# Kernel tuning notes

Measured on AMD Instinct MI355X. Metric: run time of the kernel, lower is better.

## Reference

```python
import jax, jax.numpy as jnp
import numpy as np

EPS = 1e-5   # F.instance_norm default eps
SIG = 10.0   # getGraphLap sig


def conv1(x, K):
    # x: (B, C, N), K: (O, I, kw); torch F.conv1d with 'same' padding
    p = (K.shape[-1] - 1) // 2
    return jax.lax.conv_general_dilated(
        x, K, window_strides=(1,), padding=[(p, p)],
        dimension_numbers=("NCH", "OIH", "NCH"))


def conv1T(x, K):
    # F.conv_transpose1d(x, K, padding=(kw-1)//2) == conv1d with swapped
    # in/out channels and spatially flipped kernel (stride 1, kw odd)
    Kt = jnp.flip(jnp.transpose(K, (1, 0, 2)), axis=-1)
    return conv1(x, Kt)


def avg_pool3s2(x):
    # F.avg_pool1d(x, 3, stride=2, padding=1), count_include_pad=True
    s = jax.lax.reduce_window(x, 0.0, jax.lax.add, (1, 1, 3), (1, 1, 2),
                              [(0, 0), (0, 0), (1, 1)])
    return s / 3.0


def instance_norm(z):
    mu = jnp.mean(z, axis=-1, keepdims=True)
    var = jnp.var(z, axis=-1, keepdims=True)  # biased, as in torch
    return (z - mu) * jax.lax.rsqrt(var + EPS)


def graph_lap(X, m):
    # X: (1, d, N) coords, m: (1, 1, N) mask -> (N, N) masked graph Laplacian
    Xs = X[0]                                             # (d, N)
    M = m.reshape(-1)                                     # (N,)
    Xn = Xs / (jnp.std(Xs, axis=1, keepdims=True, ddof=1) + 0.01)
    sq = jnp.sum(Xn * Xn, axis=0)                         # (N,)
    D = jnp.maximum(sq[None, :] + sq[:, None] - 2.0 * (Xn.T @ Xn), 0.0)
    We = jnp.exp(-D / SIG)
    L = jnp.diag(jnp.sum(We, axis=0)) - We
    L = jnp.outer(M, M) * L + jnp.diag(1.0 - M)
    return 0.5 * (L + L.T)


def graph_unet(x, X, m, Ks):
    xS = []
    mS = [m]
    Ls = [graph_lap(X, m)]
    # encoder / coarsening path
    for K in Ks:
        coarsen = K.shape[0] != K.shape[1]
        if coarsen:
            xS.append(x)
        z = instance_norm(mS[-1] * conv1(jnp.matmul(x, Ls[-1]), K))
        x = jax.nn.relu(z) if coarsen else x + jax.nn.relu(z)
        if coarsen:
            x = avg_pool3s2(x)
            m = avg_pool3s2(m)
            X = avg_pool3s2(X)
            mS.append(m)
            Ls.append(graph_lap(X, m))
    # decoder / refinement path
    n_scales = len(xS)
    for K in reversed(Ks):
        refine = K.shape[0] != K.shape[1]
        if refine:
            n_scales -= 1
            x = jnp.repeat(x, 2, axis=-1)  # F.interpolate nearest x2
            mS = mS[:-1]
            Ls = Ls[:-1]
        z = instance_norm(mS[-1] * conv1T(jnp.matmul(x, Ls[-1]), K))
        x = jax.nn.relu(z) if refine else x + jax.nn.relu(z)
        if refine:
            x = x + xS[n_scales]
    return x


def kernel_shapes(nLevels=3, nIn=32, nsmooth=2, stencil=9):
    shapes = []
    k = nIn
    for _ in range(nLevels):
        shapes += [(k, k, stencil)] * nsmooth
        shapes.append((2 * k, k, stencil))
        k *= 2
    shapes += [(k, k, stencil)] * nsmooth
    return shapes  # 11 kernels for (3, 32, 2)


def setup_inputs() -> dict:
    key = jax.random.key(0)
    ks = jax.random.split(key, 16)
    N = 4096
    inp = {
        "x": jax.random.normal(ks[0], (1, 32, N), jnp.float32),
        "X": jax.random.normal(ks[1], (1, 3, N), jnp.float32),
        "m": jnp.ones((1, 1, N), jnp.float32),
    }
    stdv = 1e-3
    for i, s in enumerate(kernel_shapes()):
        inp[f"K{i}"] = jax.random.uniform(ks[2 + i], s, jnp.float32, -stdv, stdv)
    return inp


def reference(x, X, m, K0, K1, K2, K3, K4, K5, K6, K7, K8, K9, K10):
    Ks = [K0, K1, K2, K3, K4, K5, K6, K7, K8, K9, K10]
    return graph_unet(x, X, m, Ks)
```

## Files before the change

kernel.cpp:

```cpp
#include <hip/hip_runtime.h>
#include <math.h>

typedef __attribute__((ext_vector_type(8))) short bf16x8;
typedef __attribute__((ext_vector_type(4))) float f32x4;

__device__ __forceinline__ ushort f2b(float f) {
    union { float f; unsigned u; } v; v.f = f;
    unsigned r = (v.u + 0x7FFFu + ((v.u >> 16) & 1u)) >> 16;
    return (ushort)r;
}
__device__ __forceinline__ float b2f(ushort h) {
    union { unsigned u; float f; } v; v.u = ((unsigned)h) << 16;
    return v.f;
}


__global__ __launch_bounds__(256) void k_prep(const float* __restrict__ X,
                                              float* __restrict__ Xn,
                                              float* __restrict__ sq, int N) {
    __shared__ double sh_s[256], sh_ss[256];
    __shared__ float sst[3];
    int t = threadIdx.x;
    for (int r = 0; r < 3; r++) {
        const float* row = X + (size_t)r * N;
        double s = 0.0, ss = 0.0;
        for (int i = t * 4; i < N; i += 1024) {
            float4 v = *(const float4*)(row + i);
            s += (double)v.x + (double)v.y + (double)v.z + (double)v.w;
            ss += (double)v.x * v.x + (double)v.y * v.y + (double)v.z * v.z + (double)v.w * v.w;
        }
        sh_s[t] = s; sh_ss[t] = ss; __syncthreads();
        for (int off = 128; off > 0; off >>= 1) {
            if (t < off) { sh_s[t] += sh_s[t + off]; sh_ss[t] += sh_ss[t + off]; }
            __syncthreads();
        }
        if (t == 0) {
            double mean = sh_s[0] / N;
            double var = (sh_ss[0] - mean * sh_s[0]) / (N - 1);
            if (var < 0.0) var = 0.0;
            sst[r] = 1.0f / ((float)sqrt(var) + 0.01f);
        }
        __syncthreads();
    }
    float s0 = sst[0], s1 = sst[1], s2 = sst[2];
    for (int i = t * 4; i < N; i += 1024) {
        float4 v0 = *(const float4*)(X + i);
        float4 v1 = *(const float4*)(X + N + i);
        float4 v2 = *(const float4*)(X + 2 * N + i);
        v0.x *= s0; v0.y *= s0; v0.z *= s0; v0.w *= s0;
        v1.x *= s1; v1.y *= s1; v1.z *= s1; v1.w *= s1;
        v2.x *= s2; v2.y *= s2; v2.z *= s2; v2.w *= s2;
        *(float4*)(Xn + i) = v0;
        *(float4*)(Xn + N + i) = v1;
        *(float4*)(Xn + 2 * N + i) = v2;
        float4 sv;
        sv.x = v0.x * v0.x + v1.x * v1.x + v2.x * v2.x;
        sv.y = v0.y * v0.y + v1.y * v1.y + v2.y * v2.y;
        sv.z = v0.z * v0.z + v1.z * v1.z + v2.z * v2.z;
        sv.w = v0.w * v0.w + v1.w * v1.w + v2.w * v2.w;
        *(float4*)(sq + i) = sv;
    }
}

template<int CPT>
__global__ __launch_bounds__(256) void k_lap(const float* __restrict__ Xn,
                                             const float* __restrict__ sq,
                                             const float* __restrict__ m,
                                             ushort* __restrict__ L, int N) {
    int i = blockIdx.x;
    int t = threadIdx.x;
    int T = blockDim.x;
    float a0 = Xn[i], a1 = Xn[N + i], a2 = Xn[2 * N + i];
    float si = sq[i];
    int j0 = t * CPT;
    float w[CPT];
    float psum = 0.f;
    #pragma unroll
    for (int q4 = 0; q4 < CPT / 4; q4++) {
        int j = j0 + q4 * 4;
        float4 x0 = *(const float4*)(Xn + j);
        float4 x1 = *(const float4*)(Xn + N + j);
        float4 x2 = *(const float4*)(Xn + 2 * N + j);
        float4 sv = *(const float4*)(sq + j);
        float D;
        D = fmaxf(si + sv.x - 2.f * (a0 * x0.x + a1 * x1.x + a2 * x2.x), 0.f);
        w[q4 * 4 + 0] = exp2f(-D * 0.14426950408889634f);
        D = fmaxf(si + sv.y - 2.f * (a0 * x0.y + a1 * x1.y + a2 * x2.y), 0.f);
        w[q4 * 4 + 1] = exp2f(-D * 0.14426950408889634f);
        D = fmaxf(si + sv.z - 2.f * (a0 * x0.z + a1 * x1.z + a2 * x2.z), 0.f);
        w[q4 * 4 + 2] = exp2f(-D * 0.14426950408889634f);
        D = fmaxf(si + sv.w - 2.f * (a0 * x0.w + a1 * x1.w + a2 * x2.w), 0.f);
        w[q4 * 4 + 3] = exp2f(-D * 0.14426950408889634f);
        psum += w[q4 * 4] + w[q4 * 4 + 1] + w[q4 * 4 + 2] + w[q4 * 4 + 3];
    }
    __shared__ float red[256];
    red[t] = psum; __syncthreads();
    for (int off = T >> 1; off > 0; off >>= 1) {
        if (t < off) red[t] += red[t + off];
        __syncthreads();
    }
    float d = red[0];
    float mi = m[i];
    ushort* Lo = L + (size_t)i * N + j0;
    #pragma unroll
    for (int q4 = 0; q4 < CPT / 4; q4++) {
        int j = j0 + q4 * 4;
        float4 mj = *(const float4*)(m + j);
        ushort o[4];
        float lv;
        lv = ((j + 0 == i) ? d : 0.f) - w[q4 * 4 + 0]; lv = mi * mj.x * lv; if (j + 0 == i) lv += 1.f - mj.x; o[0] = f2b(lv);
        lv = ((j + 1 == i) ? d : 0.f) - w[q4 * 4 + 1]; lv = mi * mj.y * lv; if (j + 1 == i) lv += 1.f - mj.y; o[1] = f2b(lv);
        lv = ((j + 2 == i) ? d : 0.f) - w[q4 * 4 + 2]; lv = mi * mj.z * lv; if (j + 2 == i) lv += 1.f - mj.z; o[2] = f2b(lv);
        lv = ((j + 3 == i) ? d : 0.f) - w[q4 * 4 + 3]; lv = mi * mj.w * lv; if (j + 3 == i) lv += 1.f - mj.w; o[3] = f2b(lv);
        *(ushort4*)(Lo + q4 * 4) = make_ushort4(o[0], o[1], o[2], o[3]);
    }
}

template<int MODE>
__global__ __launch_bounds__(256) void k_mmfT(const void* __restrict__ xsrc,
                                              const ushort* __restrict__ Lb,
                                              ushort* __restrict__ yt, int N, int C) {
    __shared__ float lds[4][64][4];
    int t = threadIdx.x;
    int wv = t >> 6, l = t & 63;
    int lrow = l & 15, lk = l >> 4;
    int j0 = blockIdx.x * 16;
    int c0 = blockIdx.y * 32;

    if (blockIdx.x == 0) {
        int row = t >> 5;
        int ch = c0 + (t & 31);
        int jj = (row < 4) ? row : N + row;
        yt[(size_t)jj * C + ch] = 0;
    }

    int kquart = N >> 2;
    size_t kbase = (size_t)wv * kquart + lk * 8;
    const ushort* bp = Lb + (size_t)(j0 + lrow) * N + kbase;
    f32x4 accA = (f32x4){0.f, 0.f, 0.f, 0.f};
    f32x4 accB = (f32x4){0.f, 0.f, 0.f, 0.f};
    if (MODE == 0) {
        const ushort* apA = (const ushort*)xsrc + (size_t)(c0 + lrow) * N + kbase;
        const ushort* apB = (const ushort*)xsrc + (size_t)(c0 + 16 + lrow) * N + kbase;
        for (int k0 = 0; k0 < kquart; k0 += 32) {
            bf16x8 b = *(const bf16x8*)(bp + k0);
            bf16x8 aA = *(const bf16x8*)(apA + k0);
            bf16x8 aB = *(const bf16x8*)(apB + k0);
            accA = __builtin_amdgcn_mfma_f32_16x16x32_bf16(aA, b, accA, 0, 0, 0);
            accB = __builtin_amdgcn_mfma_f32_16x16x32_bf16(aB, b, accB, 0, 0, 0);
        }
    } else if (MODE == 1) {
        const float* apA = (const float*)xsrc + (size_t)(c0 + lrow) * N + kbase;
        const float* apB = (const float*)xsrc + (size_t)(c0 + 16 + lrow) * N + kbase;
        for (int k0 = 0; k0 < kquart; k0 += 32) {
            bf16x8 b = *(const bf16x8*)(bp + k0);
            float4 f0 = *(const float4*)(apA + k0);
            float4 f1 = *(const float4*)(apA + k0 + 4);
            bf16x8 aA;
            aA[0] = (short)f2b(f0.x); aA[1] = (short)f2b(f0.y);
            aA[2] = (short)f2b(f0.z); aA[3] = (short)f2b(f0.w);
            aA[4] = (short)f2b(f1.x); aA[5] = (short)f2b(f1.y);
            aA[6] = (short)f2b(f1.z); aA[7] = (short)f2b(f1.w);
            float4 g0 = *(const float4*)(apB + k0);
            float4 g1 = *(const float4*)(apB + k0 + 4);
            bf16x8 aB;
            aB[0] = (short)f2b(g0.x); aB[1] = (short)f2b(g0.y);
            aB[2] = (short)f2b(g0.z); aB[3] = (short)f2b(g0.w);
            aB[4] = (short)f2b(g1.x); aB[5] = (short)f2b(g1.y);
            aB[6] = (short)f2b(g1.z); aB[7] = (short)f2b(g1.w);
            accA = __builtin_amdgcn_mfma_f32_16x16x32_bf16(aA, b, accA, 0, 0, 0);
            accB = __builtin_amdgcn_mfma_f32_16x16x32_bf16(aB, b, accB, 0, 0, 0);
        }
    } else {
        const ushort* apA = (const ushort*)xsrc + (size_t)(c0 + lrow) * (N >> 1) + (kbase >> 1);
        const ushort* apB = (const ushort*)xsrc + (size_t)(c0 + 16 + lrow) * (N >> 1) + (kbase >> 1);
        for (int k0 = 0; k0 < kquart; k0 += 32) {
            bf16x8 b = *(const bf16x8*)(bp + k0);
            ushort4 v = *(const ushort4*)(apA + (k0 >> 1));
            bf16x8 aA;
            aA[0] = (short)v.x; aA[1] = (short)v.x;
            aA[2] = (short)v.y; aA[3] = (short)v.y;
            aA[4] = (short)v.z; aA[5] = (short)v.z;
            aA[6] = (short)v.w; aA[7] = (short)v.w;
            ushort4 u = *(const ushort4*)(apB + (k0 >> 1));
            bf16x8 aB;
            aB[0] = (short)u.x; aB[1] = (short)u.x;
            aB[2] = (short)u.y; aB[3] = (short)u.y;
            aB[4] = (short)u.z; aB[5] = (short)u.z;
            aB[6] = (short)u.w; aB[7] = (short)u.w;
            accA = __builtin_amdgcn_mfma_f32_16x16x32_bf16(aA, b, accA, 0, 0, 0);
            accB = __builtin_amdgcn_mfma_f32_16x16x32_bf16(aB, b, accB, 0, 0, 0);
        }
    }
    #pragma unroll
    for (int g = 0; g < 2; g++) {
        #pragma unroll
        for (int r = 0; r < 4; r++) lds[wv][l][r] = (g == 0) ? accA[r] : accB[r];
        __syncthreads();
        if (t < 64) {
            int gg = t >> 4, j16 = t & 15;
            float s0 = lds[0][t][0] + lds[1][t][0] + lds[2][t][0] + lds[3][t][0];
            float s1 = lds[0][t][1] + lds[1][t][1] + lds[2][t][1] + lds[3][t][1];
            float s2 = lds[0][t][2] + lds[1][t][2] + lds[2][t][2] + lds[3][t][2];
            float s3 = lds[0][t][3] + lds[1][t][3] + lds[2][t][3] + lds[3][t][3];
            *(ushort4*)(yt + (size_t)(j0 + j16 + 4) * C + c0 + g * 16 + gg * 4) =
                make_ushort4(f2b(s0), f2b(s1), f2b(s2), f2b(s3));
        }
        __syncthreads();
    }
}

struct WMeta {
    const float* src[11];
    unsigned long long off_f[11];
    unsigned long long off_t[11];
    int ca[11];
    int cb[11];
};

__global__ __launch_bounds__(256) void k_wprep(WMeta meta, ushort* __restrict__ Wm) {
    int which = blockIdx.y;
    int a = meta.ca[which], b = meta.cb[which];
    int tot = a * b * 9;
    int idx = blockIdx.x * 256 + threadIdx.x;
    if (idx >= tot) return;
    int t = idx % 9;
    int oi = idx / 9;
    int i = oi % b;
    int o = oi / b;
    ushort h = f2b(meta.src[which][idx]);
    Wm[meta.off_f[which] + ((size_t)t * a + o) * b + i] = h;
    Wm[meta.off_t[which] + ((size_t)(8 - t) * b + i) * a + o] = h;
}

__global__ __launch_bounds__(256) void k_convM(const ushort* __restrict__ yt,
                                               const ushort* __restrict__ Wm,
                                               float* __restrict__ zm,
                                               const float* __restrict__ m,
                                               float2* __restrict__ sp,
                                               int C_in, int C_out, int N,
                                               int iters, int NP) {
    __shared__ float lds[4][64][4];
    int t = threadIdx.x;
    int wv = t >> 6, l = t & 63;
    int prow = l & 15, kq = l >> 4;
    int p00 = blockIdx.x * 32;
    int o0 = blockIdx.y * 16;
    int per = (iters + 3) >> 2;
    int it0 = wv * per;
    int it1 = min(iters, it0 + per);
    f32x4 accA = (f32x4){0.f, 0.f, 0.f, 0.f};
    f32x4 accB = (f32x4){0.f, 0.f, 0.f, 0.f};
    for (int it = it0; it < it1; it++) {
        int ks = it / 9;
        int tp = it - ks * 9;
        int kb = ks * 32 + kq * 8;
        bf16x8 a = *(const bf16x8*)(Wm + ((size_t)tp * C_out + o0 + prow) * C_in + kb);
        bf16x8 bA = *(const bf16x8*)(yt + (size_t)(p00 + prow + tp) * C_in + kb);
        bf16x8 bB = *(const bf16x8*)(yt + (size_t)(p00 + 16 + prow + tp) * C_in + kb);
        accA = __builtin_amdgcn_mfma_f32_16x16x32_bf16(a, bA, accA, 0, 0, 0);
        accB = __builtin_amdgcn_mfma_f32_16x16x32_bf16(a, bB, accB, 0, 0, 0);
    }
    float stsum[4] = {0.f, 0.f, 0.f, 0.f}, stss[4] = {0.f, 0.f, 0.f, 0.f};
    #pragma unroll
    for (int pg = 0; pg < 2; pg++) {
        int p0 = p00 + pg * 16;
        #pragma unroll
        for (int r = 0; r < 4; r++) lds[wv][l][r] = (pg == 0) ? accA[r] : accB[r];
        __syncthreads();
        if (t < 64) {
            int g = t >> 4, j16 = t & 15;
            int j = p0 + j16;
            float mj = m[j];
            #pragma unroll
            for (int r = 0; r < 4; r++) {
                float z = lds[0][t][r] + lds[1][t][r] + lds[2][t][r] + lds[3][t][r];
                z *= mj;
                zm[(size_t)(o0 + g * 4 + r) * N + j] = z;
                float zs = z, zz = z * z;
                #pragma unroll
                for (int mask = 1; mask < 16; mask <<= 1) {
                    zs += __shfl_xor(zs, mask);
                    zz += __shfl_xor(zz, mask);
                }
                stsum[r] += zs; stss[r] += zz;
            }
        }
        __syncthreads();
    }
    if (t < 64 && (t & 15) == 0) {
        int g = t >> 4;
        #pragma unroll
        for (int r = 0; r < 4; r++)
            sp[(size_t)(o0 + g * 4 + r) * NP + blockIdx.x] = make_float2(stsum[r], stss[r]);
    }
}

__global__ __launch_bounds__(256) void k_convC2(const float* __restrict__ zm,
                                                const float2* __restrict__ sp,
                                                const float* __restrict__ res,
                                                float* __restrict__ xout,
                                                ushort* __restrict__ xob, int N, int NP) {
    int o = blockIdx.y;
    int t = threadIdx.x;
    float2 pp = (t < NP) ? sp[(size_t)o * NP + t] : make_float2(0.f, 0.f);
    __shared__ float red[256], red2[256];
    red[t] = pp.x; red2[t] = pp.y;
    __syncthreads();
    for (int off = 128; off > 0; off >>= 1) {
        if (t < off) { red[t] += red[t + off]; red2[t] += red2[t + off]; }
        __syncthreads();
    }
    float mean = red[0] / N;
    float var = fmaxf(red2[0] / N - mean * mean, 0.f);
    float rs = rsqrtf(var + 1e-5f);
    int base = blockIdx.x * 512 + t * 2;
    float2 z = *(const float2*)(zm + (size_t)o * N + base);
    float v0 = fmaxf((z.x - mean) * rs, 0.f);
    float v1 = fmaxf((z.y - mean) * rs, 0.f);
    if (res) {
        float2 r = *(const float2*)(res + (size_t)o * N + base);
        v0 += r.x; v1 += r.y;
    }
    *(float2*)(xout + (size_t)o * N + base) = make_float2(v0, v1);
    if (xob) *(ushort2*)(xob + (size_t)o * N + base) = make_ushort2(f2b(v0), f2b(v1));
}

__global__ __launch_bounds__(256) void k_poolall(const float* __restrict__ z_in,
                                                 float* __restrict__ z_out,
                                                 ushort* __restrict__ zb_out, int Cz,
                                                 const float* __restrict__ m_in, float* __restrict__ m_out,
                                                 const float* __restrict__ X_in, float* __restrict__ X_out, int Nin) {
    int No = Nin >> 1;
    int idx = blockIdx.x * 256 + threadIdx.x;
    int total = (Cz + 4) * No;
    if (idx >= total) return;
    int r = idx / No, ii = idx - r * No;
    const float* src;
    if (r < Cz) {
        src = z_in + (size_t)r * Nin;
        float a = (ii > 0) ? src[2 * ii - 1] : 0.f;
        float v = (a + src[2 * ii] + src[2 * ii + 1]) * (1.f / 3.f);
        z_out[(size_t)r * No + ii] = v;
        zb_out[(size_t)r * No + ii] = f2b(v);
    } else if (r == Cz) {
        src = m_in;
        float a = (ii > 0) ? src[2 * ii - 1] : 0.f;
        m_out[ii] = (a + src[2 * ii] + src[2 * ii + 1]) * (1.f / 3.f);
    } else {
        src = X_in + (size_t)(r - Cz - 1) * Nin;
        float a = (ii > 0) ? src[2 * ii - 1] : 0.f;
        X_out[(size_t)(r - Cz - 1) * No + ii] = (a + src[2 * ii] + src[2 * ii + 1]) * (1.f / 3.f);
    }
}


extern "C" void kernel_launch(void* const* d_in, const int* in_sizes, int n_in,
                              void* d_out, int out_size, void* d_ws, size_t ws_size,
                              hipStream_t stream) {
    (void)in_sizes; (void)n_in; (void)out_size; (void)ws_size;
    const float* x_in = (const float*)d_in[0];
    const float* X0 = (const float*)d_in[1];
    const float* m0 = (const float*)d_in[2];
    const float* Kw[11];
    for (int i = 0; i < 11; i++) Kw[i] = (const float*)d_in[3 + i];
    float* out = (float*)d_out;
    float* ws = (float*)d_ws;

    const int Ns[4] = {4096, 2048, 1024, 512};
    const int KA[11] = {32, 32, 64, 64, 64, 128, 128, 128, 256, 256, 256};
    const int KB[11] = {32, 32, 32, 64, 64, 64, 128, 128, 128, 256, 256};

    size_t off = 0;
    auto alloc = [&](size_t n) { float* p = ws + off; off += (n + 63) & ~(size_t)63; return p; };
    ushort* Lb[4];
    Lb[0] = (ushort*)alloc(8388608); Lb[1] = (ushort*)alloc(2097152);
    Lb[2] = (ushort*)alloc(524288);  Lb[3] = (ushort*)alloc(131072);
    float* Xnb = alloc(3 * 4096);
    float* sqb = alloc(4096);
    float* spbuf = alloc(32768);
    float* zmbuf = alloc(262144);
    float* mlev[4];
    mlev[0] = const_cast<float*>(m0);
    mlev[1] = alloc(2048); mlev[2] = alloc(1024); mlev[3] = alloc(512);
    float* Xlev[4];
    Xlev[0] = const_cast<float*>(X0);
    Xlev[1] = alloc(3 * 2048); Xlev[2] = alloc(3 * 1024); Xlev[3] = alloc(3 * 512);
    float* pA[4], *pB[4], *xs[3];
    for (int l = 0; l < 4; l++) { pA[l] = alloc(131072); pB[l] = alloc(131072); }
    for (int l = 0; l < 3; l++) xs[l] = alloc(131072);
    float* zbig = alloc(262144);
    ushort* pAb[4], *pBb[4], *xsb[3];
    for (int l = 0; l < 4; l++) { pAb[l] = (ushort*)alloc(65536); pBb[l] = (ushort*)alloc(65536); }
    for (int l = 0; l < 3; l++) xsb[l] = (ushort*)alloc(65536);
    ushort* ytb = (ushort*)alloc(140000);
    ushort* Wm = (ushort*)alloc(1960000);

    size_t woff_f[11], woff_t[11];
    {
        size_t acc = 0;
        for (int k = 0; k < 11; k++) { woff_f[k] = acc; acc += (size_t)KA[k] * KB[k] * 9; }
        for (int k = 0; k < 11; k++) { woff_t[k] = acc; acc += (size_t)KA[k] * KB[k] * 9; }
    }

    {
        WMeta meta;
        for (int k = 0; k < 11; k++) {
            meta.src[k] = Kw[k];
            meta.off_f[k] = woff_f[k];
            meta.off_t[k] = woff_t[k];
            meta.ca[k] = KA[k];
            meta.cb[k] = KB[k];
        }
        k_wprep<<<dim3(2304, 11), 256, 0, stream>>>(meta, Wm);
    }

    auto build_lap = [&](int lvl) {
        int N = Ns[lvl];
        k_prep<<<1, 256, 0, stream>>>(Xlev[lvl], Xnb, sqb, N);
        if (N == 4096)      k_lap<16><<<N, 256, 0, stream>>>(Xnb, sqb, mlev[lvl], Lb[lvl], N);
        else if (N == 2048) k_lap<8><<<N, 256, 0, stream>>>(Xnb, sqb, mlev[lvl], Lb[lvl], N);
        else if (N == 1024) k_lap<4><<<N, 256, 0, stream>>>(Xnb, sqb, mlev[lvl], Lb[lvl], N);
        else                k_lap<4><<<N, 128, 0, stream>>>(Xnb, sqb, mlev[lvl], Lb[lvl], N);
    };

    auto matmul = [&](const void* xsrc, int C, int lvl, int mode) {
        int N = Ns[lvl];
        dim3 g(N / 16, C / 32);
        if (mode == 0)      k_mmfT<0><<<g, 256, 0, stream>>>(xsrc, Lb[lvl], ytb, N, C);
        else if (mode == 1) k_mmfT<1><<<g, 256, 0, stream>>>(xsrc, Lb[lvl], ytb, N, C);
        else                k_mmfT<2><<<g, 256, 0, stream>>>(xsrc, Lb[lvl], ytb, N, C);
    };

    auto conv = [&](int kidx, int lvl, const float* resv, float* ov, ushort* ovb,
                    int Cin, int Cout, int tr) {
        int N = Ns[lvl];
        int iters = (Cin / 32) * 9;
        int NP = N / 32;
        const ushort* wm = Wm + (tr ? woff_t[kidx] : woff_f[kidx]);
        k_convM<<<dim3(N / 32, Cout / 16), 256, 0, stream>>>(ytb, wm, zmbuf, mlev[lvl],
                                                             (float2*)spbuf, Cin, Cout, N, iters, NP);
        int NBs = N / 512;
        k_convC2<<<dim3(NBs, Cout), 256, 0, stream>>>(zmbuf, (const float2*)spbuf, resv, ov, ovb, N, NP);
    };

    auto poolall = [&](const float* z_in, float* z_out, ushort* zb_out, int Cz, int lvl_from) {
        int Nin = Ns[lvl_from];
        int No = Nin >> 1;
        int total = (Cz + 4) * No;
        k_poolall<<<(total + 255) / 256, 256, 0, stream>>>(z_in, z_out, zb_out, Cz,
                                                           mlev[lvl_from], mlev[lvl_from + 1],
                                                           Xlev[lvl_from], Xlev[lvl_from + 1], Nin);
    };

    build_lap(0);
    matmul(x_in, 32, 0, 1);    conv(0, 0, x_in, pA[0], pAb[0], 32, 32, 0);
    matmul(pAb[0], 32, 0, 0);  conv(1, 0, pA[0], xs[0], xsb[0], 32, 32, 0);
    matmul(xsb[0], 32, 0, 0);  conv(2, 0, nullptr, zbig, nullptr, 32, 64, 0);
    poolall(zbig, pA[1], pAb[1], 64, 0);
    build_lap(1);
    matmul(pAb[1], 64, 1, 0);  conv(3, 1, pA[1], pB[1], pBb[1], 64, 64, 0);
    matmul(pBb[1], 64, 1, 0);  conv(4, 1, pB[1], xs[1], xsb[1], 64, 64, 0);
    matmul(xsb[1], 64, 1, 0);  conv(5, 1, nullptr, zbig, nullptr, 64, 128, 0);
    poolall(zbig, pA[2], pAb[2], 128, 1);
    build_lap(2);
    matmul(pAb[2], 128, 2, 0); conv(6, 2, pA[2], pB[2], pBb[2], 128, 128, 0);
    matmul(pBb[2], 128, 2, 0); conv(7, 2, pB[2], xs[2], xsb[2], 128, 128, 0);
    matmul(xsb[2], 128, 2, 0); conv(8, 2, nullptr, zbig, nullptr, 128, 256, 0);
    poolall(zbig, pA[3], pAb[3], 256, 2);
    build_lap(3);
    matmul(pAb[3], 256, 3, 0); conv(9, 3, pA[3], pB[3], pBb[3], 256, 256, 0);
    matmul(pBb[3], 256, 3, 0); conv(10, 3, pB[3], pA[3], pAb[3], 256, 256, 0);

    matmul(pAb[3], 256, 3, 0); conv(10, 3, pA[3], pB[3], pBb[3], 256, 256, 1);
    matmul(pBb[3], 256, 3, 0); conv(9, 3, pB[3], pA[3], pAb[3], 256, 256, 1);

    matmul(pAb[3], 256, 2, 2); conv(8, 2, xs[2], pB[2], pBb[2], 256, 128, 1);
    matmul(pBb[2], 128, 2, 0); conv(7, 2, pB[2], pA[2], pAb[2], 128, 128, 1);
    matmul(pAb[2], 128, 2, 0); conv(6, 2, pA[2], pB[2], pBb[2], 128, 128, 1);

    matmul(pBb[2], 128, 1, 2); conv(5, 1, xs[1], pA[1], pAb[1], 128, 64, 1);
    matmul(pAb[1], 64, 1, 0);  conv(4, 1, pA[1], pB[1], pBb[1], 64, 64, 1);
    matmul(pBb[1], 64, 1, 0);  conv(3, 1, pB[1], pA[1], pAb[1], 64, 64, 1);

    matmul(pAb[1], 64, 0, 2);  conv(2, 0, xs[0], pB[0], pBb[0], 64, 32, 1);
    matmul(pBb[0], 32, 0, 0);  conv(1, 0, pB[0], pA[0], pAb[0], 32, 32, 1);
    matmul(pAb[0], 32, 0, 0);  conv(0, 0, pA[0], out, nullptr, 32, 32, 1);
}
```

Baseline: 508.2 us.

## Fuse instance-norm, ReLU and residual epilogue into the next Laplacian matmul

Adds a MODE 3 matmul variant that reduces the per-channel conv statistics, then applies instance-norm, ReLU and the residual add on the fly while loading the activation operand. The separate k_convC2 launch is skipped on residual layers at levels 1-3, and the matmul's first column block writes the fp32 activation for later residual use. This removes one kernel launch and a full activation pass per fused layer. In exchange, every block recomputes the stats and re-applies the normalization, reading fp32 z and residual instead of bf16 input, so matmul read traffic grows.

```diff
diff --git a/kernel.cpp b/kernel.cpp
--- a/kernel.cpp
+++ b/kernel.cpp
@@ -119,8 +119,13 @@
 template<int MODE>
 __global__ __launch_bounds__(256) void k_mmfT(const void* __restrict__ xsrc,
                                               const ushort* __restrict__ Lb,
-                                              ushort* __restrict__ yt, int N, int C) {
+                                              ushort* __restrict__ yt, int N, int C,
+                                              const float* __restrict__ zsrc,
+                                              const float2* __restrict__ spst,
+                                              const float* __restrict__ resv,
+                                              float* __restrict__ xw, int NP) {
     __shared__ float lds[4][64][4];
+    __shared__ float smean[32], srs[32];
     int t = threadIdx.x;
     int wv = t >> 6, l = t & 63;
     int lrow = l & 15, lk = l >> 4;
@@ -132,6 +137,19 @@
         int ch = c0 + (t & 31);
         int jj = (row < 4) ? row : N + row;
         yt[(size_t)jj * C + ch] = 0;
+    }
+
+    if (MODE == 3) {
+        if (t < 32) {
+            int ch = c0 + t;
+            const float2* pp = spst + (size_t)ch * NP;
+            float s = 0.f, ss = 0.f;
+            for (int k = 0; k < NP; k++) { float2 v = pp[k]; s += v.x; ss += v.y; }
+            float mean = s / N;
+            float var = fmaxf(ss / N - mean * mean, 0.f);
+            smean[t] = mean; srs[t] = rsqrtf(var + 1e-5f);
+        }
+        __syncthreads();
     }
 
     int kquart = N >> 2;
@@ -171,7 +189,7 @@
             accA = __builtin_amdgcn_mfma_f32_16x16x32_bf16(aA, b, accA, 0, 0, 0);
             accB = __builtin_amdgcn_mfma_f32_16x16x32_bf16(aB, b, accB, 0, 0, 0);
         }
-    } else {
+    } else if (MODE == 2) {
         const ushort* apA = (const ushort*)xsrc + (size_t)(c0 + lrow) * (N >> 1) + (kbase >> 1);
         const ushort* apB = (const ushort*)xsrc + (size_t)(c0 + 16 + lrow) * (N >> 1) + (kbase >> 1);
         for (int k0 = 0; k0 < kquart; k0 += 32) {
@@ -188,6 +206,59 @@
             aB[2] = (short)u.y; aB[3] = (short)u.y;
             aB[4] = (short)u.z; aB[5] = (short)u.z;
             aB[6] = (short)u.w; aB[7] = (short)u.w;
+            accA = __builtin_amdgcn_mfma_f32_16x16x32_bf16(aA, b, accA, 0, 0, 0);
+            accB = __builtin_amdgcn_mfma_f32_16x16x32_bf16(aB, b, accB, 0, 0, 0);
+        }
+    } else {
+        float meanA = smean[lrow], rsAv = srs[lrow];
+        float meanB = smean[16 + lrow], rsBv = srs[16 + lrow];
+        const float* zA = zsrc + (size_t)(c0 + lrow) * N + kbase;
+        const float* zB = zsrc + (size_t)(c0 + 16 + lrow) * N + kbase;
+        const float* rA = resv + (size_t)(c0 + lrow) * N + kbase;
+        const float* rB = resv + (size_t)(c0 + 16 + lrow) * N + kbase;
+        float* wA = xw + (size_t)(c0 + lrow) * N + kbase;
+        float* wB = xw + (size_t)(c0 + 16 + lrow) * N + kbase;
+        bool wr = (blockIdx.x == 0);
+        for (int k0 = 0; k0 < kquart; k0 += 32) {
+            bf16x8 b = *(const bf16x8*)(bp + k0);
+            float4 z0 = *(const float4*)(zA + k0);
+            float4 z1 = *(const float4*)(zA + k0 + 4);
+            float4 r0 = *(const float4*)(rA + k0);
+            float4 r1 = *(const float4*)(rA + k0 + 4);
+            float4 xa0, xa1;
+            xa0.x = fmaxf((z0.x - meanA) * rsAv, 0.f) + r0.x;
+            xa0.y = fmaxf((z0.y - meanA) * rsAv, 0.f) + r0.y;
+            xa0.z = fmaxf((z0.z - meanA) * rsAv, 0.f) + r0.z;
+            xa0.w = fmaxf((z0.w - meanA) * rsAv, 0.f) + r0.w;
+            xa1.x = fmaxf((z1.x - meanA) * rsAv, 0.f) + r1.x;
+            xa1.y = fmaxf((z1.y - meanA) * rsAv, 0.f) + r1.y;
+            xa1.z = fmaxf((z1.z - meanA) * rsAv, 0.f) + r1.z;
+            xa1.w = fmaxf((z1.w - meanA) * rsAv, 0.f) + r1.w;
+            if (wr) { *(float4*)(wA + k0) = xa0; *(float4*)(wA + k0 + 4) = xa1; }
+            bf16x8 aA;
+            aA[0] = (short)f2b(xa0.x); aA[1] = (short)f2b(xa0.y);
+            aA[2] = (short)f2b(xa0.z); aA[3] = (short)f2b(xa0.w);
+            aA[4] = (short)f2b(xa1.x); aA[5] = (short)f2b(xa1.y);
+            aA[6] = (short)f2b(xa1.z); aA[7] = (short)f2b(xa1.w);
+            float4 u0 = *(const float4*)(zB + k0);
+            float4 u1 = *(const float4*)(zB + k0 + 4);
+            float4 s0 = *(const float4*)(rB + k0);
+            float4 s1 = *(const float4*)(rB + k0 + 4);
+            float4 xb0, xb1;
+            xb0.x = fmaxf((u0.x - meanB) * rsBv, 0.f) + s0.x;
+            xb0.y = fmaxf((u0.y - meanB) * rsBv, 0.f) + s0.y;
+            xb0.z = fmaxf((u0.z - meanB) * rsBv, 0.f) + s0.z;
+            xb0.w = fmaxf((u0.w - meanB) * rsBv, 0.f) + s0.w;
+            xb1.x = fmaxf((u1.x - meanB) * rsBv, 0.f) + s1.x;
+            xb1.y = fmaxf((u1.y - meanB) * rsBv, 0.f) + s1.y;
+            xb1.z = fmaxf((u1.z - meanB) * rsBv, 0.f) + s1.z;
+            xb1.w = fmaxf((u1.w - meanB) * rsBv, 0.f) + s1.w;
+            if (wr) { *(float4*)(wB + k0) = xb0; *(float4*)(wB + k0 + 4) = xb1; }
+            bf16x8 aB;
+            aB[0] = (short)f2b(xb0.x); aB[1] = (short)f2b(xb0.y);
+            aB[2] = (short)f2b(xb0.z); aB[3] = (short)f2b(xb0.w);
+            aB[4] = (short)f2b(xb1.x); aB[5] = (short)f2b(xb1.y);
+            aB[6] = (short)f2b(xb1.z); aB[7] = (short)f2b(xb1.w);
             accA = __builtin_amdgcn_mfma_f32_16x16x32_bf16(aA, b, accA, 0, 0, 0);
             accB = __builtin_amdgcn_mfma_f32_16x16x32_bf16(aB, b, accB, 0, 0, 0);
         }
@@ -427,21 +498,31 @@
     auto matmul = [&](const void* xsrc, int C, int lvl, int mode) {
         int N = Ns[lvl];
         dim3 g(N / 16, C / 32);
-        if (mode == 0)      k_mmfT<0><<<g, 256, 0, stream>>>(xsrc, Lb[lvl], ytb, N, C);
-        else if (mode == 1) k_mmfT<1><<<g, 256, 0, stream>>>(xsrc, Lb[lvl], ytb, N, C);
-        else                k_mmfT<2><<<g, 256, 0, stream>>>(xsrc, Lb[lvl], ytb, N, C);
+        if (mode == 0)      k_mmfT<0><<<g, 256, 0, stream>>>(xsrc, Lb[lvl], ytb, N, C, nullptr, nullptr, nullptr, nullptr, 0);
+        else if (mode == 1) k_mmfT<1><<<g, 256, 0, stream>>>(xsrc, Lb[lvl], ytb, N, C, nullptr, nullptr, nullptr, nullptr, 0);
+        else                k_mmfT<2><<<g, 256, 0, stream>>>(xsrc, Lb[lvl], ytb, N, C, nullptr, nullptr, nullptr, nullptr, 0);
     };
 
+    auto matmul3 = [&](const float* resv, float* xw, int C, int lvl) {
+        int N = Ns[lvl];
+        int NP = N / 32;
+        dim3 g(N / 16, C / 32);
+        k_mmfT<3><<<g, 256, 0, stream>>>(nullptr, Lb[lvl], ytb, N, C,
+                                         zmbuf, (const float2*)spbuf, resv, xw, NP);
+    };
+
     auto conv = [&](int kidx, int lvl, const float* resv, float* ov, ushort* ovb,
-                    int Cin, int Cout, int tr) {
+                    int Cin, int Cout, int tr, bool doC2) {
         int N = Ns[lvl];
         int iters = (Cin / 32) * 9;
         int NP = N / 32;
         const ushort* wm = Wm + (tr ? woff_t[kidx] : woff_f[kidx]);
         k_convM<<<dim3(N / 32, Cout / 16), 256, 0, stream>>>(ytb, wm, zmbuf, mlev[lvl],
                                                              (float2*)spbuf, Cin, Cout, N, iters, NP);
-        int NBs = N / 512;
-        k_convC2<<<dim3(NBs, Cout), 256, 0, stream>>>(zmbuf, (const float2*)spbuf, resv, ov, ovb, N, NP);
+        if (doC2) {
+            int NBs = N / 512;
+            k_convC2<<<dim3(NBs, Cout), 256, 0, stream>>>(zmbuf, (const float2*)spbuf, resv, ov, ovb, N, NP);
+        }
     };
 
     auto poolall = [&](const float* z_in, float* z_out, ushort* zb_out, int Cz, int lvl_from) {
@@ -454,36 +535,36 @@
     };
 
     build_lap(0);
-    matmul(x_in, 32, 0, 1);    conv(0, 0, x_in, pA[0], pAb[0], 32, 32, 0);
-    matmul(pAb[0], 32, 0, 0);  conv(1, 0, pA[0], xs[0], xsb[0], 32, 32, 0);
-    matmul(xsb[0], 32, 0, 0);  conv(2, 0, nullptr, zbig, nullptr, 32, 64, 0);
+    matmul(x_in, 32, 0, 1);    conv(0, 0, x_in, pA[0], pAb[0], 32, 32, 0, true);
+    matmul(pAb[0], 32, 0, 0);  conv(1, 0, pA[0], xs[0], xsb[0], 32, 32, 0, true);
+    matmul(xsb[0], 32, 0, 0);  conv(2, 0, nullptr, zbig, nullptr, 32, 64, 0, true);
     poolall(zbig, pA[1], pAb[1], 64, 0);
     build_lap(1);
-    matmul(pAb[1], 64, 1, 0);  conv(3, 1, pA[1], pB[1], pBb[1], 64, 64, 0);
-    matmul(pBb[1], 64, 1, 0);  conv(4, 1, pB[1], xs[1], xsb[1], 64, 64, 0);
-    matmul(xsb[1], 64, 1, 0);  conv(5, 1, nullptr, zbig, nullptr, 64, 128, 0);
+    matmul(pAb[1], 64, 1, 0);        conv(3, 1, nullptr, nullptr, nullptr, 64, 64, 0, false);
+    matmul3(pA[1], pB[1], 64, 1);    conv(4, 1, nullptr, nullptr, nullptr, 64, 64, 0, false);
+    matmul3(pB[1], xs[1], 64, 1);    conv(5, 1, nullptr, zbig, nullptr, 64, 128, 0, true);
     poolall(zbig, pA[2], pAb[2], 128, 1);
     build_lap(2);
-    matmul(pAb[2], 128, 2, 0); conv(6, 2, pA[2], pB[2], pBb[2], 128, 128, 0);
-    matmul(pBb[2], 128, 2, 0); conv(7, 2, pB[2], xs[2], xsb[2], 128, 128, 0);
-    matmul(xsb[2], 128, 2, 0); conv(8, 2, nullptr, zbig, nullptr, 128, 256, 0);
+    matmul(pAb[2], 128, 2, 0);       conv(6, 2, nullptr, nullptr, nullptr, 128, 128, 0, false);
+    matmul3(pA[2], pB[2], 128, 2);   conv(7, 2, nullptr, nullptr, nullptr, 128, 128, 0, false);
+    matmul3(pB[2], xs[2], 128, 2);   conv(8, 2, nullptr, zbig, nullptr, 128, 256, 0, true);
     poolall(zbig, pA[3], pAb[3], 256, 2);
     build_lap(3);
-    matmul(pAb[3], 256, 3, 0); conv(9, 3, pA[3], pB[3], pBb[3], 256, 256, 0);
-    matmul(pBb[3], 256, 3, 0); conv(10, 3, pB[3], pA[3], pAb[3], 256, 256, 0);
-
-    matmul(pAb[3], 256, 3, 0); conv(10, 3, pA[3], pB[3], pBb[3], 256, 256, 1);
-    matmul(pBb[3], 256, 3, 0); conv(9, 3, pB[3], pA[3], pAb[3], 256, 256, 1);
-
-    matmul(pAb[3], 256, 2, 2); conv(8, 2, xs[2], pB[2], pBb[2], 256, 128, 1);
-    matmul(pBb[2], 128, 2, 0); conv(7, 2, pB[2], pA[2], pAb[2], 128, 128, 1);
-    matmul(pAb[2], 128, 2, 0); conv(6, 2, pA[2], pB[2], pBb[2], 128, 128, 1);
-
-    matmul(pBb[2], 128, 1, 2); conv(5, 1, xs[1], pA[1], pAb[1], 128, 64, 1);
-    matmul(pAb[1], 64, 1, 0);  conv(4, 1, pA[1], pB[1], pBb[1], 64, 64, 1);
-    matmul(pBb[1], 64, 1, 0);  conv(3, 1, pB[1], pA[1], pAb[1], 64, 64, 1);
-
-    matmul(pAb[1], 64, 0, 2);  conv(2, 0, xs[0], pB[0], pBb[0], 64, 32, 1);
-    matmul(pBb[0], 32, 0, 0);  conv(1, 0, pB[0], pA[0], pAb[0], 32, 32, 1);
-    matmul(pAb[0], 32, 0, 0);  conv(0, 0, pA[0], out, nullptr, 32, 32, 1);
-}
+    matmul(pAb[3], 256, 3, 0);       conv(9, 3, nullptr, nullptr, nullptr, 256, 256, 0, false);
+    matmul3(pA[3], pB[3], 256, 3);   conv(10, 3, nullptr, nullptr, nullptr, 256, 256, 0, false);
+
+    matmul3(pB[3], pA[3], 256, 3);   conv(10, 3, nullptr, nullptr, nullptr, 256, 256, 1, false);
+    matmul3(pA[3], pB[3], 256, 3);   conv(9, 3, pB[3], pA[3], pAb[3], 256, 256, 1, true);
+
+    matmul(pAb[3], 256, 2, 2);       conv(8, 2, nullptr, nullptr, nullptr, 256, 128, 1, false);
+    matmul3(xs[2], pB[2], 128, 2);   conv(7, 2, nullptr, nullptr, nullptr, 128, 128, 1, false);
+    matmul3(pB[2], pA[2], 128, 2);   conv(6, 2, pA[2], pB[2], pBb[2], 128, 128, 1, true);
+
+    matmul(pBb[2], 128, 1, 2);       conv(5, 1, nullptr, nullptr, nullptr, 128, 64, 1, false);
+    matmul3(xs[1], pA[1], 64, 1);    conv(4, 1, nullptr, nullptr, nullptr, 64, 64, 1, false);
+    matmul3(pA[1], pB[1], 64, 1);    conv(3, 1, pB[1], pA[1], pAb[1], 64, 64, 1, true);
+
+    matmul(pAb[1], 64, 0, 2);        conv(2, 0, xs[0], pB[0], pBb[0], 64, 32, 1, true);
+    matmul(pBb[0], 32, 0, 0);        conv(1, 0, pB[0], pA[0], pAb[0], 32, 32, 1, true);
+    matmul(pAb[0], 32, 0, 0);        conv(0, 0, pA[0], out, nullptr, 32, 32, 1, true);
+}
```

Result: slower. 613.1 us (+20.6%).
